# Optimization experiments

Measured on AMD Instinct MI355X. Metric: run time of the kernel, lower is better.

The kernel has to match this reference:

```python
import jax, jax.numpy as jnp
import numpy as np

NEG_SLOPE = 0.2


def add_self_loops(edge_index, num_nodes):
    loop = jnp.arange(num_nodes, dtype=edge_index.dtype)
    loops = jnp.stack([loop, loop])  # [2, N]
    return jnp.concatenate([edge_index, loops], axis=1)


def gat_conv(x, edge_index, W, a_src, a_dst, b, concat=True):
    """PyG-style GATConv. a_src/a_dst: [1, H, C]. W: [F_in, H*C]."""
    N = x.shape[0]
    H, C = a_src.shape[1], a_src.shape[2]
    xp = (x @ W).reshape(N, H, C)                       # [N, H, C]
    alpha_src = (xp * a_src).sum(-1)                    # [N, H]
    alpha_dst = (xp * a_dst).sum(-1)                    # [N, H]
    src, dst = edge_index[0], edge_index[1]
    e = alpha_src[src] + alpha_dst[dst]                 # [E, H]
    e = jnp.where(e > 0, e, NEG_SLOPE * e)              # LeakyReLU(0.2)
    # per-destination segment softmax
    m = jax.ops.segment_max(e, dst, num_segments=N)     # [N, H]
    m = jnp.where(jnp.isfinite(m), m, 0.0)
    ez = jnp.exp(e - m[dst])
    s = jax.ops.segment_sum(ez, dst, num_segments=N)    # [N, H]
    alpha = ez / (s[dst] + 1e-16)                       # [E, H]
    msg = xp[src] * alpha[:, :, None]                   # [E, H, C]
    out = jax.ops.segment_sum(msg, dst, num_segments=N) # [N, H, C]
    out = out.reshape(N, H * C) if concat else out.mean(axis=1)
    return out + b


def setup_inputs() -> dict:
    key = jax.random.key(0)
    ks = jax.random.split(key, 16)
    N, F, E, CLS = 100000, 256, 1600000, 10
    x = jax.random.normal(ks[0], (N, F), dtype=jnp.float32)
    edge_index = jax.random.randint(ks[1], (2, E), 0, N, dtype=jnp.int64)

    def glorot(k, shape):
        fan = shape[0] + shape[-1] * (shape[1] if len(shape) == 3 else 1)
        return jax.random.uniform(k, shape, jnp.float32, -1.0, 1.0) * jnp.sqrt(6.0 / fan)

    return {
        "x": x, "edge_index": edge_index,
        "W1": glorot(ks[2], (F, 128)),  "a1s": glorot(ks[3], (1, 8, 16)),
        "a1d": glorot(ks[4], (1, 8, 16)), "b1": jnp.zeros((128,), jnp.float32),
        "W2": glorot(ks[5], (128, 64)), "a2s": glorot(ks[6], (1, 8, 8)),
        "a2d": glorot(ks[7], (1, 8, 8)),  "b2": jnp.zeros((64,), jnp.float32),
        "W3": glorot(ks[8], (64, CLS)), "a3s": glorot(ks[9], (1, 1, CLS)),
        "a3d": glorot(ks[10], (1, 1, CLS)), "b3": jnp.zeros((CLS,), jnp.float32),
    }


def reference(x, edge_index, W1, a1s, a1d, b1, W2, a2s, a2d, b2, W3, a3s, a3d, b3):
    ei = add_self_loops(edge_index, x.shape[0])
    h = jax.nn.elu(gat_conv(x, ei, W1, a1s, a1d, b1))
    h = jax.nn.elu(gat_conv(h, ei, W2, a2s, a2d, b2))
    h = gat_conv(h, ei, W3, a3s, a3d, b3)
    return jax.nn.log_softmax(h, axis=1)
```

## Files before the change

kernel.cpp:

```cpp
#include <hip/hip_runtime.h>
#include <hip/hip_bf16.h>
#include <math.h>


#define LEAKY(v) ((v) > 0.f ? (v) : 0.2f * (v))

typedef __bf16 bf16_t;
typedef __bf16 bf16x8 __attribute__((ext_vector_type(8)));
typedef __bf16 bf16x4 __attribute__((ext_vector_type(4)));
typedef float f32x4 __attribute__((ext_vector_type(4)));
typedef unsigned short u16x8 __attribute__((ext_vector_type(8)));

static __device__ __forceinline__ unsigned short bf_bits(float f) {
    bf16_t b = (bf16_t)f;
    return __builtin_bit_cast(unsigned short, b);
}
static __device__ __forceinline__ float bf_to_f(unsigned short u) {
    return __uint_as_float(((unsigned int)u) << 16);
}
static __device__ __forceinline__ float bperm_f(int byteaddr, float v) {
    return __uint_as_float((unsigned)__builtin_amdgcn_ds_bpermute(byteaddr, (int)__float_as_uint(v)));
}

constexpr int NB_MAX = 400;
constexpr int BCAP = 5120;

__global__ void zero_k(int* a, int n) {
    int i = blockIdx.x * blockDim.x + threadIdx.x;
    if (i < n) a[i] = 0;
}

__global__ __launch_bounds__(256) void partition_k(
        const int* __restrict__ src, const int* __restrict__ dst, int E, int NB,
        int* __restrict__ bcur, unsigned* __restrict__ staged) {
    __shared__ int hist[NB_MAX];
    __shared__ int bstart[NB_MAX + 1];
    __shared__ int cur[NB_MAX];
    __shared__ int gbase[NB_MAX];
    __shared__ unsigned words[4096];
    __shared__ unsigned short bidl[4096];
    int tid = threadIdx.x;
    int e0 = blockIdx.x * 4096;
    int cnt = E - e0; if (cnt > 4096) cnt = 4096;
    if (cnt <= 0) return;

    for (int b = tid; b < NB; b += 256) hist[b] = 0;
    __syncthreads();
    for (int i = tid; i < cnt; i += 256) atomicAdd(&hist[dst[e0 + i] >> 8], 1);
    __syncthreads();
    if (tid == 0) {
        int run = 0;
        for (int b = 0; b < NB; b++) { bstart[b] = run; run += hist[b]; }
        bstart[NB] = run;
    }
    __syncthreads();
    for (int b = tid; b < NB; b += 256) {
        cur[b] = bstart[b];
        gbase[b] = hist[b] ? atomicAdd(&bcur[b], hist[b]) : 0;
    }
    __syncthreads();
    for (int i = tid; i < cnt; i += 256) {
        int s = src[e0 + i], d = dst[e0 + i];
        int b = d >> 8;
        unsigned w = (unsigned)s | ((unsigned)(d & 255) << 17);
        int p = atomicAdd(&cur[b], 1);
        words[p] = w;
        bidl[p] = (unsigned short)b;
    }
    __syncthreads();
    for (int i = tid; i < cnt; i += 256) {
        int b = bidl[i];
        staged[(size_t)b * BCAP + gbase[b] + (i - bstart[b])] = words[i];
    }
}

__global__ void scan_nb_k(const int* __restrict__ bcur, int* __restrict__ ebase, int NB) {
    int lane = threadIdx.x;
    int CH = (NB + 63) / 64;
    int b0 = lane * CH;
    int v[8]; int s = 0;
#pragma unroll 8
    for (int k = 0; k < CH; k++) { int b = b0 + k; int t = (b < NB) ? bcur[b] : 0; if (k < 8) v[k] = t; s += t; }
    int orig = s;
    for (int off = 1; off < 64; off <<= 1) {
        int t = __shfl_up(s, off, 64);
        if (lane >= off) s += t;
    }
    int run = s - orig;
    for (int k = 0; k < CH; k++) { int b = b0 + k; if (b < NB) { ebase[b] = run; run += v[k]; } }
    if (lane == 63) ebase[NB] = run;
}

__global__ __launch_bounds__(256) void buildcsr_k(
        const unsigned* __restrict__ staged, const int* __restrict__ bcur,
        const int* __restrict__ ebase, int* __restrict__ offs, int* __restrict__ cols,
        int N, int NB) {
    __shared__ int h[256], hs[256], curl[256];
    __shared__ int colsl[BCAP];
    int b = blockIdx.x, tid = threadIdx.x;
    int n0 = b << 8;
    int ecnt = bcur[b];
    int base_g = ebase[b];
    const unsigned* sb = staged + (size_t)b * BCAP;

    h[tid] = 0;
    __syncthreads();
    for (int i = tid; i < ecnt; i += 256) atomicAdd(&h[sb[i] >> 17], 1);
    __syncthreads();
    int val = h[tid];
    hs[tid] = val; __syncthreads();
    for (int off = 1; off < 256; off <<= 1) {
        int t = (tid >= off) ? hs[tid - off] : 0;
        __syncthreads();
        hs[tid] += t;
        __syncthreads();
    }
    int excl = hs[tid] - val;
    curl[tid] = excl;
    if (n0 + tid < N) offs[n0 + tid] = base_g + excl;
    if (b == NB - 1 && tid == 0) offs[N] = base_g + ecnt;
    __syncthreads();
    for (int i = tid; i < ecnt; i += 256) {
        unsigned w = sb[i];
        int p = atomicAdd(&curl[w >> 17], 1);
        colsl[p] = (int)(w & 0x1FFFFu);
    }
    __syncthreads();
    for (int i = tid; i < ecnt; i += 256) cols[base_g + i] = colsl[i];
}

__global__ void prep_w_k(const float* __restrict__ W, short* __restrict__ Bfs,
                         int K, int N, int NT, int total) {
    int idx = blockIdx.x * blockDim.x + threadIdx.x;
    if (idx >= total) return;
    int lane = idx & 63;
    int t = idx >> 6;
    int ntile = t % NT, kstep = t / NT;
    int quad = lane >> 4, nl = lane & 15;
    int n = ntile * 16 + nl;
    bf16_t* dst = (bf16_t*)Bfs + (size_t)idx * 16;
#pragma unroll
    for (int j = 0; j < 8; j++) {
        int k = kstep * 32 + quad * 8 + j;
        float v = W[k * N + n];
        bf16_t h = (bf16_t)v;
        bf16_t l = (bf16_t)(v - (float)h);
        dst[j] = h;
        dst[8 + j] = l;
    }
}

template <int BM, int WMT, int WNT, int NWM, bool ABF16, int CHEAD, int K>
__global__ __launch_bounds__(256, 2) void mfma_gemm_k(
        const void* __restrict__ Av, const short* __restrict__ Bfs,
        unsigned short* __restrict__ Cb,
        const float* __restrict__ a_s, const float* __restrict__ a_d,
        float* __restrict__ out_as, float* __restrict__ out_ad,
        int M, int N, int NT) {
    constexpr int NWN = 4 / NWM;
    constexpr int BN = 16 * WNT * NWN;
    constexpr int KP = K + 8;
    __shared__ __align__(16) bf16_t As_hi[BM * KP];
    __shared__ __align__(16) bf16_t As_lo[ABF16 ? 16 : BM * KP];
    const bf16_t* Bf = (const bf16_t*)Bfs;

    int tid = threadIdx.x;
    int wave = tid >> 6, lane = tid & 63;
    int quad = lane >> 4, l16 = lane & 15;
    int wm = wave % NWM, wn = wave / NWM;
    int row0 = blockIdx.x * BM;
    int ntile0 = blockIdx.y * (BN / 16) + wn * WNT;

    if constexpr (!ABF16) {
        constexpr int CHUNKS = BM * K * 4 / (16 * 256);
        const float* A = (const float*)Av;
        f32x4 tmp[CHUNKS];
#pragma unroll
        for (int c = 0; c < CHUNKS; c++) {
            int ci = c * 256 + tid;
            int fi = ci * 4;
            int row = fi / K, k = fi % K;
            int grow = row0 + row;
            tmp[c] = (f32x4){0.f, 0.f, 0.f, 0.f};
            if (grow < M) tmp[c] = *(const f32x4*)(A + (size_t)grow * K + k);
        }
#pragma unroll
        for (int c = 0; c < CHUNKS; c++) {
            int ci = c * 256 + tid;
            int fi = ci * 4;
            int row = fi / K, k = fi % K;
            bf16x4 h, l;
#pragma unroll
            for (int j = 0; j < 4; j++) {
                bf16_t hh = (bf16_t)tmp[c][j];
                h[j] = hh;
                l[j] = (bf16_t)(tmp[c][j] - (float)hh);
            }
            *(bf16x4*)&As_hi[row * KP + k] = h;
            *(bf16x4*)&As_lo[row * KP + k] = l;
        }
    } else {
        constexpr int CHUNKS = BM * K * 2 / (16 * 256);
        const unsigned short* A = (const unsigned short*)Av;
        u16x8 tmp[CHUNKS];
#pragma unroll
        for (int c = 0; c < CHUNKS; c++) {
            int ci = c * 256 + tid;
            int ei = ci * 8;
            int row = ei / K, k = ei % K;
            int grow = row0 + row;
            tmp[c] = (u16x8){0, 0, 0, 0, 0, 0, 0, 0};
            if (grow < M) tmp[c] = *(const u16x8*)(A + (size_t)grow * K + k);
        }
#pragma unroll
        for (int c = 0; c < CHUNKS; c++) {
            int ci = c * 256 + tid;
            int ei = ci * 8;
            int row = ei / K, k = ei % K;
            *(u16x8*)&As_hi[row * KP + k] = tmp[c];
        }
    }
    __syncthreads();

    f32x4 acc[WMT][WNT];
#pragma unroll
    for (int i = 0; i < WMT; i++)
#pragma unroll
        for (int j = 0; j < WNT; j++) acc[i][j] = (f32x4){0.f, 0.f, 0.f, 0.f};

#pragma unroll
    for (int ks = 0; ks < K / 32; ks++) {
        bf16x8 ah[WMT], al[WMT];
#pragma unroll
        for (int i = 0; i < WMT; i++) {
            int rowl = wm * (WMT * 16) + i * 16 + l16;
            ah[i] = *(const bf16x8*)&As_hi[rowl * KP + ks * 32 + quad * 8];
            if (!ABF16) al[i] = *(const bf16x8*)&As_lo[rowl * KP + ks * 32 + quad * 8];
        }
        bf16x8 bh[WNT], bl[WNT];
#pragma unroll
        for (int j = 0; j < WNT; j++) {
            size_t base = ((size_t)(ks * NT + ntile0 + j) * 64 + lane) * 16;
            bh[j] = *(const bf16x8*)&Bf[base];
            bl[j] = *(const bf16x8*)&Bf[base + 8];
        }
#pragma unroll
        for (int i = 0; i < WMT; i++)
#pragma unroll
            for (int j = 0; j < WNT; j++) {
                acc[i][j] = __builtin_amdgcn_mfma_f32_16x16x32_bf16(ah[i], bh[j], acc[i][j], 0, 0, 0);
                if (!ABF16)
                    acc[i][j] = __builtin_amdgcn_mfma_f32_16x16x32_bf16(al[i], bh[j], acc[i][j], 0, 0, 0);
                acc[i][j] = __builtin_amdgcn_mfma_f32_16x16x32_bf16(ah[i], bl[j], acc[i][j], 0, 0, 0);
            }
    }

#pragma unroll
    for (int i = 0; i < WMT; i++) {
        int rbase = row0 + wm * (WMT * 16) + i * 16 + quad * 4;
#pragma unroll
        for (int j = 0; j < WNT; j++) {
            int gcol = (ntile0 + j) * 16 + l16;
#pragma unroll
            for (int r2 = 0; r2 < 4; r2++) {
                int grow = rbase + r2;
                if (grow < M) Cb[(size_t)grow * N + gcol] = bf_bits(acc[i][j][r2]);
            }
        }
    }

    const int Hh = N / CHEAD;
#pragma unroll
    for (int j = 0; j < WNT; j++) {
        int gcol = (ntile0 + j) * 16 + l16;
        float cs = a_s[gcol], cd = a_d[gcol];
#pragma unroll
        for (int i = 0; i < WMT; i++) {
            float ps[4], pd[4];
#pragma unroll
            for (int r2 = 0; r2 < 4; r2++) {
                ps[r2] = acc[i][j][r2] * cs;
                pd[r2] = acc[i][j][r2] * cd;
            }
#pragma unroll
            for (int off = 1; off < CHEAD; off <<= 1) {
#pragma unroll
                for (int r2 = 0; r2 < 4; r2++) {
                    ps[r2] += __shfl_xor(ps[r2], off, 64);
                    pd[r2] += __shfl_xor(pd[r2], off, 64);
                }
            }
            if ((l16 & (CHEAD - 1)) == 0) {
                int hd = gcol / CHEAD;
                int rb = row0 + wm * (WMT * 16) + i * 16 + quad * 4;
#pragma unroll
                for (int r2 = 0; r2 < 4; r2++) {
                    int grow = rb + r2;
                    if (grow < M) {
                        out_as[(size_t)grow * Hh + hd] = ps[r2];
                        out_ad[(size_t)grow * Hh + hd] = pd[r2];
                    }
                }
            }
        }
    }
}

template <int BM, int BN, int BK, int TM, int TN>
__global__ void gemm_k(const unsigned short* __restrict__ Ab, const float* __restrict__ B,
                       float* __restrict__ C, unsigned short* __restrict__ Cb,
                       int M, int Nc, int K) {
    __shared__ float As[BK][BM + 1];
    __shared__ float Bs[BK][BN + 1];
    int tx = threadIdx.x, ty = threadIdx.y;
    int tid = ty * blockDim.x + tx;
    const int nthreads = (BM / TM) * (BN / TN);
    int row0 = blockIdx.x * BM, col0 = blockIdx.y * BN;
    float acc[TM][TN];
#pragma unroll
    for (int i = 0; i < TM; i++)
#pragma unroll
        for (int j = 0; j < TN; j++) acc[i][j] = 0.f;

    for (int k0 = 0; k0 < K; k0 += BK) {
        for (int i = tid; i < BM * BK; i += nthreads) {
            int r = i / BK, kk = i % BK;
            int gr = row0 + r;
            As[kk][r] = (gr < M) ? bf_to_f(Ab[(size_t)gr * K + (k0 + kk)]) : 0.f;
        }
        for (int i = tid; i < BK * BN; i += nthreads) {
            int kk = i / BN, c = i % BN;
            int gc = col0 + c;
            Bs[kk][c] = (gc < Nc) ? B[(long)(k0 + kk) * Nc + gc] : 0.f;
        }
        __syncthreads();
#pragma unroll
        for (int kk = 0; kk < BK; ++kk) {
            float a[TM], b[TN];
#pragma unroll
            for (int i = 0; i < TM; i++) a[i] = As[kk][ty * TM + i];
#pragma unroll
            for (int j = 0; j < TN; j++) b[j] = Bs[kk][tx * TN + j];
#pragma unroll
            for (int i = 0; i < TM; i++)
#pragma unroll
                for (int j = 0; j < TN; j++) acc[i][j] = fmaf(a[i], b[j], acc[i][j]);
        }
        __syncthreads();
    }
#pragma unroll
    for (int i = 0; i < TM; i++) {
        int gr = row0 + ty * TM + i;
        if (gr >= M) continue;
#pragma unroll
        for (int j = 0; j < TN; j++) {
            int gc = col0 + tx * TN + j;
            if (gc < Nc) {
                C[(long)gr * Nc + gc] = acc[i][j];
                Cb[(long)gr * Nc + gc] = bf_bits(acc[i][j]);
            }
        }
    }
}

template <int H, int C>
__global__ void alpha_k(const float* __restrict__ xp, const float* __restrict__ a_s,
                        const float* __restrict__ a_d, float* __restrict__ out_s,
                        float* __restrict__ out_d, int NH) {
    int i = blockIdx.x * blockDim.x + threadIdx.x;
    if (i >= NH) return;
    int h = i % H;
    const float* v = xp + (long)i * C;
    float ss = 0.f, sd = 0.f;
#pragma unroll
    for (int c = 0; c < C; c++) {
        float x = v[c];
        ss = fmaf(x, a_s[h * C + c], ss);
        sd = fmaf(x, a_d[h * C + c], sd);
    }
    out_s[i] = ss;
    out_d[i] = sd;
}

template <bool DO_ELU>
__global__ void agg16_k(const unsigned short* __restrict__ xpb,
                        const float* __restrict__ asrc, const float* __restrict__ adst,
                        const int* __restrict__ offs, const int* __restrict__ cols,
                        const float* __restrict__ bias, unsigned short* __restrict__ outb,
                        int N) {
    int gtid = blockIdx.x * blockDim.x + threadIdx.x;
    int n = gtid >> 6;
    if (n >= N) return;
    int lane = threadIdx.x & 63;
    int j = lane >> 3, h = lane & 7;
    const int jb = j << 2;
    int start = offs[n], end = offs[n + 1];
    const unsigned* xp32 = (const unsigned*)xpb;

    float ad_l = adst[n * 8 + h];
    float vs = asrc[n * 8 + h] + ad_l;
    vs = LEAKY(vs);

    float m_w = vs;
    float s = (j == 0) ? 1.f : 0.f;
    float m_f = bperm_f(jb, vs);
    unsigned uself = xp32[(size_t)n * 64 + lane];
    float a0 = __uint_as_float(uself << 16);
    float a1 = __uint_as_float(uself & 0xffff0000u);

    for (int c0 = start; c0 < end; c0 += 8) {
        int e = c0 + j;
        bool valid = e < end;
        int src_l = valid ? cols[e] : 0;
        float v = -1e30f;
        if (valid) {
            v = asrc[src_l * 8 + h] + ad_l;
            v = LEAKY(v);
        }
        float cm = v;
        cm = fmaxf(cm, __shfl_xor(cm, 8, 64));
        cm = fmaxf(cm, __shfl_xor(cm, 16, 64));
        cm = fmaxf(cm, __shfl_xor(cm, 32, 64));
        float mw_new = fmaxf(m_w, cm);
        float w_raw = __expf(v - mw_new);
        s = s * __expf(m_w - mw_new) + w_raw;
        m_w = mw_new;
        float cmF = bperm_f(jb, cm);
        float mf_new = fmaxf(m_f, cmF);
        float scF = __expf(m_f - mf_new);
        m_f = mf_new;
        a0 *= scF; a1 *= scF;
#pragma unroll
        for (int j2 = 0; j2 < 8; j2++) {
            int srcj = __builtin_amdgcn_readlane(src_l, j2 * 8);
            float w = bperm_f(jb + j2 * 32, w_raw);
            unsigned u = xp32[(size_t)srcj * 64 + lane];
            a0 = fmaf(w, __uint_as_float(u << 16), a0);
            a1 = fmaf(w, __uint_as_float(u & 0xffff0000u), a1);
        }
    }
    s += __shfl_xor(s, 8, 64);
    s += __shfl_xor(s, 16, 64);
    s += __shfl_xor(s, 32, 64);
    float rs = 1.f / (s + 1e-16f);
    float rsF = bperm_f(jb, rs);
    float o0 = a0 * rsF + bias[2 * lane];
    float o1 = a1 * rsF + bias[2 * lane + 1];
    if (DO_ELU) {
        o0 = o0 > 0.f ? o0 : __expf(o0) - 1.f;
        o1 = o1 > 0.f ? o1 : __expf(o1) - 1.f;
    }
    unsigned packed = (unsigned)bf_bits(o0) | ((unsigned)bf_bits(o1) << 16);
    ((unsigned*)outb)[(size_t)n * 64 + lane] = packed;
}

template <bool DO_ELU>
__global__ void agg8c8_k(const unsigned short* __restrict__ xpb,
                         const float* __restrict__ asrc, const float* __restrict__ adst,
                         const int* __restrict__ offs, const int* __restrict__ cols,
                         const float* __restrict__ bias, unsigned short* __restrict__ outb,
                         int N) {
    int gtid = blockIdx.x * blockDim.x + threadIdx.x;
    int n = gtid >> 6;
    if (n >= N) return;
    int lane = threadIdx.x & 63;
    int j = lane >> 3, h = lane & 7;
    int start = offs[n], end = offs[n + 1];
    const unsigned* xp32 = (const unsigned*)xpb;

    int fp = lane & 31;
    int hF = fp >> 2;
    int half = lane >> 5;
    int sbase = half * 32;

    float ad_l = adst[n * 8 + h];
    float vs = asrc[n * 8 + h] + ad_l;
    vs = LEAKY(vs);

    float m_w = vs;
    float s = (j == 0) ? 1.f : 0.f;
    float m_f = bperm_f(hF * 4, vs);
    float a0 = 0.f, a1 = 0.f;
    if (half == 0) {
        unsigned u = xp32[(size_t)n * 32 + fp];
        a0 = __uint_as_float(u << 16);
        a1 = __uint_as_float(u & 0xffff0000u);
    }

    for (int c0 = start; c0 < end; c0 += 8) {
        int e = c0 + j;
        bool valid = e < end;
        int src_l = valid ? cols[e] : 0;
        float v = -1e30f;
        if (valid) {
            v = asrc[src_l * 8 + h] + ad_l;
            v = LEAKY(v);
        }
        float cm = v;
        cm = fmaxf(cm, __shfl_xor(cm, 8, 64));
        cm = fmaxf(cm, __shfl_xor(cm, 16, 64));
        cm = fmaxf(cm, __shfl_xor(cm, 32, 64));
        float mw_new = fmaxf(m_w, cm);
        float w_raw = __expf(v - mw_new);
        s = s * __expf(m_w - mw_new) + w_raw;
        m_w = mw_new;
        float cmF = bperm_f(hF * 4, cm);
        float mf_new = fmaxf(m_f, cmF);
        float scF = __expf(m_f - mf_new);
        m_f = mf_new;
        a0 *= scF; a1 *= scF;
#pragma unroll
        for (int j2 = 0; j2 < 4; j2++) {
            int srcv = __builtin_amdgcn_ds_bpermute(sbase + j2 * 64, src_l);
            float w = bperm_f(sbase + hF * 4 + j2 * 64, w_raw);
            unsigned u = xp32[(size_t)srcv * 32 + fp];
            a0 = fmaf(w, __uint_as_float(u << 16), a0);
            a1 = fmaf(w, __uint_as_float(u & 0xffff0000u), a1);
        }
    }
    s += __shfl_xor(s, 8, 64);
    s += __shfl_xor(s, 16, 64);
    s += __shfl_xor(s, 32, 64);
    float rs = 1.f / (s + 1e-16f);
    float rsF = bperm_f(hF * 4, rs);
    a0 += __shfl_xor(a0, 32, 64);
    a1 += __shfl_xor(a1, 32, 64);
    if (half == 0) {
        float o0 = a0 * rsF + bias[2 * fp];
        float o1 = a1 * rsF + bias[2 * fp + 1];
        if (DO_ELU) {
            o0 = o0 > 0.f ? o0 : __expf(o0) - 1.f;
            o1 = o1 > 0.f ? o1 : __expf(o1) - 1.f;
        }
        unsigned packed = (unsigned)bf_bits(o0) | ((unsigned)bf_bits(o1) << 16);
        ((unsigned*)outb)[(size_t)n * 32 + fp] = packed;
    }
}

__global__ void agg1h_k(const unsigned short* __restrict__ xpb,
                        const float* __restrict__ asrc, const float* __restrict__ adst,
                        const int* __restrict__ offs, const int* __restrict__ cols,
                        const float* __restrict__ bias, float* __restrict__ out, int N) {
    int gtid = blockIdx.x * blockDim.x + threadIdx.x;
    int n = gtid >> 6;
    if (n >= N) return;
    int lane = threadIdx.x & 63;
    int start = offs[n], end = offs[n + 1];
    float ad = adst[n];
    float vs = asrc[n] + ad;
    vs = LEAKY(vs);

    float m, s;
    if (lane == 0) { m = vs; s = 1.f; } else { m = -1e30f; s = 0.f; }
    for (int e = start + lane; e < end; e += 64) {
        float v = asrc[cols[e]] + ad;
        v = LEAKY(v);
        float mo = fmaxf(m, v);
        s = s * __expf(m - mo) + __expf(v - mo);
        m = mo;
    }
#pragma unroll
    for (int off = 1; off <= 32; off <<= 1) {
        float mo = __shfl_xor(m, off, 64);
        float so = __shfl_xor(s, off, 64);
        float mn = fmaxf(m, mo);
        s = s * __expf(m - mn) + so * __expf(mo - mn);
        m = mn;
    }
    float rs = 1.f / (s + 1e-16f);
    float wself = __expf(vs - m) * rs;

    int j = lane / 10, c = lane - j * 10;
    float acc = 0.f;
    if (j == 0) acc = wself * bf_to_f(xpb[(size_t)n * 10 + c]);
    for (int c0 = start; c0 < end; c0 += 6) {
        int e = c0 + j;
        if (j < 6 && e < end) {
            int src = cols[e];
            float v = asrc[src] + ad;
            v = LEAKY(v);
            float w = __expf(v - m) * rs;
            acc = fmaf(w, bf_to_f(xpb[(size_t)src * 10 + c]), acc);
        }
    }
    float tot = acc;
#pragma unroll
    for (int k = 1; k < 6; k++) tot += __shfl(acc, lane + 10 * k, 64);

    float z = tot + bias[lane < 10 ? lane : 0];
    float mx = -1e30f;
#pragma unroll
    for (int k = 0; k < 10; k++) mx = fmaxf(mx, __shfl(z, k, 64));
    float se = 0.f;
#pragma unroll
    for (int k = 0; k < 10; k++) se += __expf(__shfl(z, k, 64) - mx);
    if (lane < 10) out[(size_t)n * 10 + lane] = z - (__logf(se) + mx);
}


static inline size_t alignup(size_t x) { return (x + 255) & ~(size_t)255; }

extern "C" void kernel_launch(void* const* d_in, const int* in_sizes, int n_in,
                              void* d_out, int out_size, void* d_ws, size_t ws_size,
                              hipStream_t stream) {
    const float* x   = (const float*)d_in[0];
    const int*   ei  = (const int*)d_in[1];
    const float* W1  = (const float*)d_in[2];
    const float* a1s = (const float*)d_in[3];
    const float* a1d = (const float*)d_in[4];
    const float* b1  = (const float*)d_in[5];
    const float* W2  = (const float*)d_in[6];
    const float* a2s = (const float*)d_in[7];
    const float* a2d = (const float*)d_in[8];
    const float* b2  = (const float*)d_in[9];
    const float* W3  = (const float*)d_in[10];
    const float* a3s = (const float*)d_in[11];
    const float* a3d = (const float*)d_in[12];
    const float* b3  = (const float*)d_in[13];
    float* out = (float*)d_out;

    const int N = in_sizes[0] / 256;
    const int E = in_sizes[1] / 2;
    const int* src = ei;
    const int* dst = ei + E;
    const int NB = (N + 255) >> 8;

    char* p = (char*)d_ws;
    int* offs    = (int*)p; p += alignup(sizeof(int) * (size_t)(N + 1));
    int* bcur    = (int*)p; p += alignup(sizeof(int) * (size_t)(NB_MAX + 1));
    int* ebase   = (int*)p; p += alignup(sizeof(int) * (size_t)(NB_MAX + 1));
    int* cols    = (int*)p; p += alignup(sizeof(int) * (size_t)E);
    unsigned short* xpb   = (unsigned short*)p; p += alignup(2 * (size_t)N * 128);
    unsigned short* hbufb = (unsigned short*)p; p += alignup(2 * (size_t)N * 128);
    float* xp    = (float*)p; p += alignup(sizeof(float) * (size_t)N * 128);
    float* as_   = (float*)p; p += alignup(sizeof(float) * (size_t)N * 8);
    float* ad_   = (float*)p; p += alignup(sizeof(float) * (size_t)N * 8);
    short* Bf1   = (short*)p; p += alignup(sizeof(short) * 8 * 8 * 64 * 16);
    short* Bf2   = (short*)p; p += alignup(sizeof(short) * 4 * 4 * 64 * 16);
    unsigned* staged = (unsigned*)xp;

    const int TB = 256;

    zero_k<<<(NB + TB - 1) / TB, TB, 0, stream>>>(bcur, NB);
    partition_k<<<(E + 4095) / 4096, 256, 0, stream>>>(src, dst, E, NB, bcur, staged);
    scan_nb_k<<<1, 64, 0, stream>>>(bcur, ebase, NB);
    buildcsr_k<<<NB, 256, 0, stream>>>(staged, bcur, ebase, offs, cols, N, NB);

    prep_w_k<<<(4096 + TB - 1) / TB, TB, 0, stream>>>(W1, Bf1, 256, 128, 8, 4096);
    prep_w_k<<<(1024 + TB - 1) / TB, TB, 0, stream>>>(W2, Bf2, 128, 64, 4, 1024);

    mfma_gemm_k<64, 4, 2, 1, false, 16, 256><<<dim3((N + 63) / 64, 1), 256, 0, stream>>>(
        x, Bf1, xpb, a1s, a1d, as_, ad_, N, 128, 8);
    agg16_k<true><<<(N * 64 + TB - 1) / TB, TB, 0, stream>>>(
        xpb, as_, ad_, offs, cols, b1, hbufb, N);

    mfma_gemm_k<64, 4, 1, 1, true, 8, 128><<<dim3((N + 63) / 64, 1), 256, 0, stream>>>(
        hbufb, Bf2, xpb, a2s, a2d, as_, ad_, N, 64, 4);
    agg8c8_k<true><<<(N * 64 + TB - 1) / TB, TB, 0, stream>>>(
        xpb, as_, ad_, offs, cols, b2, hbufb, N);

    gemm_k<64, 16, 16, 4, 1><<<dim3((N + 63) / 64, 1), dim3(16, 16), 0, stream>>>(
        hbufb, W3, xp, xpb, N, 10, 64);
    alpha_k<1, 10><<<(N + TB - 1) / TB, TB, 0, stream>>>(xp, a3s, a3d, as_, ad_, N);
    agg1h_k<<<(N * 64 + TB - 1) / TB, TB, 0, stream>>>(
        xpb, as_, ad_, offs, cols, b3, out, N);
}
```

Before: 520.0 us.

## Split online softmax into max/sum pass then rescale-free aggregation pass

The two 8-head aggregation kernels now make a first pass over each node's edges to find the per-head max and the exp-sum. A second pass then gathers and accumulates the bf16 features with final weights, so the accumulators no longer need rescaling each chunk. Both passes process 16 edges per iteration to raise memory-level parallelism. In exchange, the cols and asrc gathers and the exp computations are done twice, which adds index and logit traffic in return for a shorter dependency chain in the feature loop.

```diff
diff --git a/kernel.cpp b/kernel.cpp
--- a/kernel.cpp
+++ b/kernel.cpp
@@ -403,47 +403,62 @@
 
     float m_w = vs;
     float s = (j == 0) ? 1.f : 0.f;
-    float m_f = bperm_f(jb, vs);
-    unsigned uself = xp32[(size_t)n * 64 + lane];
-    float a0 = __uint_as_float(uself << 16);
-    float a1 = __uint_as_float(uself & 0xffff0000u);
-
-    for (int c0 = start; c0 < end; c0 += 8) {
-        int e = c0 + j;
-        bool valid = e < end;
-        int src_l = valid ? cols[e] : 0;
-        float v = -1e30f;
-        if (valid) {
-            v = asrc[src_l * 8 + h] + ad_l;
-            v = LEAKY(v);
-        }
-        float cm = v;
+    for (int c0 = start; c0 < end; c0 += 16) {
+        int e0 = c0 + j, e1 = c0 + 8 + j;
+        bool ok0 = e0 < end, ok1 = e1 < end;
+        int s0 = ok0 ? cols[e0] : 0;
+        int s1 = ok1 ? cols[e1] : 0;
+        float v0 = -1e30f, v1 = -1e30f;
+        if (ok0) { v0 = asrc[s0 * 8 + h] + ad_l; v0 = LEAKY(v0); }
+        if (ok1) { v1 = asrc[s1 * 8 + h] + ad_l; v1 = LEAKY(v1); }
+        float cm = fmaxf(v0, v1);
         cm = fmaxf(cm, __shfl_xor(cm, 8, 64));
         cm = fmaxf(cm, __shfl_xor(cm, 16, 64));
         cm = fmaxf(cm, __shfl_xor(cm, 32, 64));
         float mw_new = fmaxf(m_w, cm);
-        float w_raw = __expf(v - mw_new);
-        s = s * __expf(m_w - mw_new) + w_raw;
+        s = s * __expf(m_w - mw_new) + __expf(v0 - mw_new) + __expf(v1 - mw_new);
         m_w = mw_new;
-        float cmF = bperm_f(jb, cm);
-        float mf_new = fmaxf(m_f, cmF);
-        float scF = __expf(m_f - mf_new);
-        m_f = mf_new;
-        a0 *= scF; a1 *= scF;
-#pragma unroll
-        for (int j2 = 0; j2 < 8; j2++) {
-            int srcj = __builtin_amdgcn_readlane(src_l, j2 * 8);
-            float w = bperm_f(jb + j2 * 32, w_raw);
-            unsigned u = xp32[(size_t)srcj * 64 + lane];
-            a0 = fmaf(w, __uint_as_float(u << 16), a0);
-            a1 = fmaf(w, __uint_as_float(u & 0xffff0000u), a1);
-        }
     }
     s += __shfl_xor(s, 8, 64);
     s += __shfl_xor(s, 16, 64);
     s += __shfl_xor(s, 32, 64);
     float rs = 1.f / (s + 1e-16f);
+
+    float mF = bperm_f(jb, m_w);
     float rsF = bperm_f(jb, rs);
+
+    unsigned uself = xp32[(size_t)n * 64 + lane];
+    float wsF = __expf(bperm_f(jb, vs) - mF);
+    float a0 = wsF * __uint_as_float(uself << 16);
+    float a1 = wsF * __uint_as_float(uself & 0xffff0000u);
+
+    for (int c0 = start; c0 < end; c0 += 16) {
+        int e0 = c0 + j, e1 = c0 + 8 + j;
+        bool ok0 = e0 < end, ok1 = e1 < end;
+        int sl0 = ok0 ? cols[e0] : 0;
+        int sl1 = ok1 ? cols[e1] : 0;
+        float v0 = -1e30f, v1 = -1e30f;
+        if (ok0) { v0 = asrc[sl0 * 8 + h] + ad_l; v0 = LEAKY(v0); }
+        if (ok1) { v1 = asrc[sl1 * 8 + h] + ad_l; v1 = LEAKY(v1); }
+        float w0 = __expf(v0 - m_w);
+        float w1 = __expf(v1 - m_w);
+#pragma unroll
+        for (int j2 = 0; j2 < 8; j2++) {
+            int srcj = __builtin_amdgcn_readlane(sl0, j2 * 8);
+            float w = bperm_f(jb + j2 * 32, w0);
+            unsigned u = xp32[(size_t)srcj * 64 + lane];
+            a0 = fmaf(w, __uint_as_float(u << 16), a0);
+            a1 = fmaf(w, __uint_as_float(u & 0xffff0000u), a1);
+        }
+#pragma unroll
+        for (int j2 = 0; j2 < 8; j2++) {
+            int srcj = __builtin_amdgcn_readlane(sl1, j2 * 8);
+            float w = bperm_f(jb + j2 * 32, w1);
+            unsigned u = xp32[(size_t)srcj * 64 + lane];
+            a0 = fmaf(w, __uint_as_float(u << 16), a0);
+            a1 = fmaf(w, __uint_as_float(u & 0xffff0000u), a1);
+        }
+    }
     float o0 = a0 * rsF + bias[2 * lane];
     float o1 = a1 * rsF + bias[2 * lane + 1];
     if (DO_ELU) {
@@ -479,50 +494,65 @@
 
     float m_w = vs;
     float s = (j == 0) ? 1.f : 0.f;
-    float m_f = bperm_f(hF * 4, vs);
-    float a0 = 0.f, a1 = 0.f;
-    if (half == 0) {
-        unsigned u = xp32[(size_t)n * 32 + fp];
-        a0 = __uint_as_float(u << 16);
-        a1 = __uint_as_float(u & 0xffff0000u);
-    }
-
-    for (int c0 = start; c0 < end; c0 += 8) {
-        int e = c0 + j;
-        bool valid = e < end;
-        int src_l = valid ? cols[e] : 0;
-        float v = -1e30f;
-        if (valid) {
-            v = asrc[src_l * 8 + h] + ad_l;
-            v = LEAKY(v);
-        }
-        float cm = v;
+    for (int c0 = start; c0 < end; c0 += 16) {
+        int e0 = c0 + j, e1 = c0 + 8 + j;
+        bool ok0 = e0 < end, ok1 = e1 < end;
+        int s0 = ok0 ? cols[e0] : 0;
+        int s1 = ok1 ? cols[e1] : 0;
+        float v0 = -1e30f, v1 = -1e30f;
+        if (ok0) { v0 = asrc[s0 * 8 + h] + ad_l; v0 = LEAKY(v0); }
+        if (ok1) { v1 = asrc[s1 * 8 + h] + ad_l; v1 = LEAKY(v1); }
+        float cm = fmaxf(v0, v1);
         cm = fmaxf(cm, __shfl_xor(cm, 8, 64));
         cm = fmaxf(cm, __shfl_xor(cm, 16, 64));
         cm = fmaxf(cm, __shfl_xor(cm, 32, 64));
         float mw_new = fmaxf(m_w, cm);
-        float w_raw = __expf(v - mw_new);
-        s = s * __expf(m_w - mw_new) + w_raw;
+        s = s * __expf(m_w - mw_new) + __expf(v0 - mw_new) + __expf(v1 - mw_new);
         m_w = mw_new;
-        float cmF = bperm_f(hF * 4, cm);
-        float mf_new = fmaxf(m_f, cmF);
-        float scF = __expf(m_f - mf_new);
-        m_f = mf_new;
-        a0 *= scF; a1 *= scF;
-#pragma unroll
-        for (int j2 = 0; j2 < 4; j2++) {
-            int srcv = __builtin_amdgcn_ds_bpermute(sbase + j2 * 64, src_l);
-            float w = bperm_f(sbase + hF * 4 + j2 * 64, w_raw);
-            unsigned u = xp32[(size_t)srcv * 32 + fp];
-            a0 = fmaf(w, __uint_as_float(u << 16), a0);
-            a1 = fmaf(w, __uint_as_float(u & 0xffff0000u), a1);
-        }
     }
     s += __shfl_xor(s, 8, 64);
     s += __shfl_xor(s, 16, 64);
     s += __shfl_xor(s, 32, 64);
     float rs = 1.f / (s + 1e-16f);
+
+    float mF = bperm_f(hF * 4, m_w);
     float rsF = bperm_f(hF * 4, rs);
+
+    float a0 = 0.f, a1 = 0.f;
+    if (half == 0) {
+        float wsF = __expf(bperm_f(hF * 4, vs) - mF);
+        unsigned u = xp32[(size_t)n * 32 + fp];
+        a0 = wsF * __uint_as_float(u << 16);
+        a1 = wsF * __uint_as_float(u & 0xffff0000u);
+    }
+
+    for (int c0 = start; c0 < end; c0 += 16) {
+        int e0 = c0 + j, e1 = c0 + 8 + j;
+        bool ok0 = e0 < end, ok1 = e1 < end;
+        int sl0 = ok0 ? cols[e0] : 0;
+        int sl1 = ok1 ? cols[e1] : 0;
+        float v0 = -1e30f, v1 = -1e30f;
+        if (ok0) { v0 = asrc[sl0 * 8 + h] + ad_l; v0 = LEAKY(v0); }
+        if (ok1) { v1 = asrc[sl1 * 8 + h] + ad_l; v1 = LEAKY(v1); }
+        float w0 = __expf(v0 - m_w);
+        float w1 = __expf(v1 - m_w);
+#pragma unroll
+        for (int j2 = 0; j2 < 4; j2++) {
+            int srcv = __builtin_amdgcn_ds_bpermute(sbase + j2 * 64, sl0);
+            float w = bperm_f(sbase + hF * 4 + j2 * 64, w0);
+            unsigned u = xp32[(size_t)srcv * 32 + fp];
+            a0 = fmaf(w, __uint_as_float(u << 16), a0);
+            a1 = fmaf(w, __uint_as_float(u & 0xffff0000u), a1);
+        }
+#pragma unroll
+        for (int j2 = 0; j2 < 4; j2++) {
+            int srcv = __builtin_amdgcn_ds_bpermute(sbase + j2 * 64, sl1);
+            float w = bperm_f(sbase + hF * 4 + j2 * 64, w1);
+            unsigned u = xp32[(size_t)srcv * 32 + fp];
+            a0 = fmaf(w, __uint_as_float(u << 16), a0);
+            a1 = fmaf(w, __uint_as_float(u & 0xffff0000u), a1);
+        }
+    }
     a0 += __shfl_xor(a0, 32, 64);
     a1 += __shfl_xor(a1, 32, 64);
     if (half == 0) {
```

Result: slower. 540.0 us (+3.8%).
